# Kernel tuning notes

Hardware: AMD Instinct MI355X
Metric: run time of the kernel (lower is better)

Reference implementation:

```python
import jax, jax.numpy as jnp
import numpy as np

B, S, D, H, DF, L, NC, V, U = 1024, 50, 96, 8, 192, 3, 3, 40000, 5000


def layernorm(x, g, b, eps=1e-5):
    m = jnp.mean(x, axis=-1, keepdims=True)
    v = jnp.mean((x - m) ** 2, axis=-1, keepdims=True)
    return (x - m) * jax.lax.rsqrt(v + eps) * g + b


def gelu(x):
    return jax.nn.gelu(x, approximate=False)  # torch nn.GELU default (erf)


def mha(q, k, v, wi, bi, wo, bo, h):
    # torch nn.MultiheadAttention (batch_first): packed in_proj then out_proj
    d = q.shape[-1]
    dh = d // h
    qp = q @ wi[:d].T + bi[:d]
    kp = k @ wi[d:2 * d].T + bi[d:2 * d]
    vp = v @ wi[2 * d:].T + bi[2 * d:]
    qh = qp.reshape(qp.shape[0], qp.shape[1], h, dh)
    kh = kp.reshape(kp.shape[0], kp.shape[1], h, dh)
    vh = vp.reshape(vp.shape[0], vp.shape[1], h, dh)
    s = jnp.einsum('bqhd,bkhd->bhqk', qh, kh) * (1.0 / np.sqrt(dh)).astype(np.float32)
    a = jax.nn.softmax(s, axis=-1)
    o = jnp.einsum('bhqk,bkhd->bqhd', a, vh).reshape(qp.shape[0], qp.shape[1], d)
    return o @ wo.T + bo


def setup_inputs():
    key = jax.random.key(0)
    ks = iter(jax.random.split(key, 64))

    def p(shape, s=0.02):
        return jax.random.normal(next(ks), shape, jnp.float32) * s

    inp = {
        'locations': jax.random.randint(next(ks), (B, S), 0, V),
        'users': jax.random.randint(next(ks), (B, S), 0, U),
        'start_mins': jax.random.randint(next(ks), (B, S), 0, 1440),
        'weekdays': jax.random.randint(next(ks), (B, S), 0, 7),
        'loc_emb': p((V, D)), 'user_emb': p((U, D)),
        'hour_emb': p((24, D // 4)), 'wd_emb': p((7, D // 4)),
        'temp_w': p((D, D // 2)), 'temp_b': jnp.zeros((D,), jnp.float32),
        'pos_embed': p((1, S, D)), 'init_hidden': p((D,)),
        'out_w1': p((D, D)), 'out_b1': jnp.zeros((D,), jnp.float32),
        'out_w2': p((V, D)), 'out_b2': jnp.zeros((V,), jnp.float32),
    }
    for pre in ('sa', 'ci', 'ch'):  # self_attn, cross_attn_input, cross_attn_hidden
        inp[pre + '_wi'] = p((L, 3 * D, D))
        inp[pre + '_bi'] = jnp.zeros((L, 3 * D), jnp.float32)
        inp[pre + '_wo'] = p((L, D, D))
        inp[pre + '_bo'] = jnp.zeros((L, D), jnp.float32)
    inp['ffn_w1'] = p((L, DF, D)); inp['ffn_b1'] = jnp.zeros((L, DF), jnp.float32)
    inp['ffn_w2'] = p((L, D, DF)); inp['ffn_b2'] = jnp.zeros((L, D), jnp.float32)
    inp['gate_w'] = p((L, D, 2 * D)); inp['gate_b'] = jnp.zeros((L, D), jnp.float32)
    for n in ('n1', 'n2', 'n3'):
        inp[n + '_g'] = jnp.ones((L, D), jnp.float32)
        inp[n + '_b'] = jnp.zeros((L, D), jnp.float32)
    return inp


def reference(locations, users, start_mins, weekdays,
              loc_emb, user_emb, hour_emb, wd_emb, temp_w, temp_b,
              pos_embed, init_hidden, out_w1, out_b1, out_w2, out_b2,
              sa_wi, sa_bi, sa_wo, sa_bo, ci_wi, ci_bi, ci_wo, ci_bo,
              ch_wi, ch_bi, ch_wo, ch_bo, ffn_w1, ffn_b1, ffn_w2, ffn_b2,
              gate_w, gate_b, n1_g, n1_b, n2_g, n2_b, n3_g, n3_b):
    b, s = locations.shape
    hours = (start_mins // 60) % 24
    temporal = jnp.concatenate([hour_emb[hours], wd_emb[weekdays]], axis=-1)  # (B,S,D//2)
    x = (loc_emb[locations] + user_emb[users[:, 0]][:, None, :]
         + temporal @ temp_w.T + temp_b + pos_embed[:, :s, :])  # (B,S,D)
    hidden = jnp.broadcast_to(init_hidden, (b, D))
    for _cycle in range(NC):
        for l in range(L):
            attn = mha(x, x, x, sa_wi[l], sa_bi[l], sa_wo[l], sa_bo[l], H)
            a1 = layernorm(attn + x, n1_g[l], n1_b[l])
            he = hidden[:, None, :]  # single-token query (B,1,D)
            c1 = mha(he, a1, a1, ci_wi[l], ci_bi[l], ci_wo[l], ci_bo[l], H)[:, 0]
            c2 = mha(he, he, he, ch_wi[l], ch_bi[l], ch_wo[l], ch_bo[l], H)[:, 0]
            g = jax.nn.sigmoid(jnp.concatenate([c1, c2], axis=-1) @ gate_w[l].T + gate_b[l])
            gated = layernorm(g * c1 + (1.0 - g) * c2 + hidden, n2_g[l], n2_b[l])
            f = gelu(gated @ ffn_w1[l].T + ffn_b1[l]) @ ffn_w2[l].T + ffn_b2[l]
            hidden = layernorm(f + gated, n3_g[l], n3_b[l])
    logits = gelu(hidden @ out_w1.T + out_b1) @ out_w2.T + out_b2  # (B,V)
    return logits
```

## Files before the change

### kernel.cpp

```cpp
#include <hip/hip_runtime.h>
#include <math.h>

#define B_ 1024
#define S_ 50
#define D_ 96
#define H_ 8
#define DH_ 12
#define DF_ 192
#define L_ 3
#define NC_ 3
#define V_ 40000
#define SR_ 4

#define SCR_L 14745600ull
#define KV_L  9830400ull

typedef __attribute__((ext_vector_type(8))) short short8v;
typedef __attribute__((ext_vector_type(4))) float float4v;

__device__ __forceinline__ float dot4f(float4 a, float4 b) {
  return a.x*b.x + a.y*b.y + a.z*b.z + a.w*b.w;
}
__device__ __forceinline__ float geluf(float v) {
  return 0.5f*v*(1.0f + erff(v*0.70710678118654752f));
}

__global__ void k_embed(const int* __restrict__ loc, const int* __restrict__ users,
                        const int* __restrict__ mins, const int* __restrict__ wd,
                        const float* __restrict__ loc_emb, const float* __restrict__ user_emb,
                        const float* __restrict__ hour_emb, const float* __restrict__ wd_emb,
                        const float* __restrict__ temp_w, const float* __restrict__ temp_b,
                        const float* __restrict__ pos, float* __restrict__ x)
{
  int bs = blockIdx.x; int b = bs / S_; int s = bs % S_;
  __shared__ float tmp[48];
  int t = threadIdx.x;
  if (t < 48) {
    int hr = (mins[bs] / 60) % 24;
    int w  = wd[bs];
    tmp[t] = (t < 24) ? hour_emb[hr*24 + t] : wd_emb[w*24 + (t-24)];
  }
  __syncthreads();
  int lc = loc[bs]; int u = users[b*S_];
  float acc = temp_b[t] + loc_emb[(size_t)lc*D_ + t] + user_emb[(size_t)u*D_ + t] + pos[s*D_ + t];
  const float* twr = temp_w + t*48;
  #pragma unroll
  for (int k = 0; k < 48; k++) acc += tmp[k] * twr[k];
  x[(size_t)bs*D_ + t] = acc;
}

__global__ void k_init(const float* __restrict__ init_hidden, float* __restrict__ hidden) {
  int i = blockIdx.x*256 + threadIdx.x;
  if (i < B_*D_) hidden[i] = init_hidden[i % D_];
}

__global__ void k_tobf16(const float* __restrict__ in, unsigned short* __restrict__ out, int n) {
  int i = blockIdx.x*256 + threadIdx.x;
  if (i < n) {
    unsigned int b = __float_as_uint(in[i]);
    unsigned int r = (b + 0x7FFFu + ((b >> 16) & 1u)) >> 16;
    out[i] = (unsigned short)r;
  }
}

__global__ __launch_bounds__(256) void k_qkv_mfma(const unsigned short* __restrict__ xb,
                                                  const unsigned short* __restrict__ wib,
                                                  const float* __restrict__ bi_b,
                                                  float* __restrict__ qkv)
{
  int l = blockIdx.y;
  const unsigned short* wi = wib + (size_t)l*288*96;
  const float* bi = bi_b + (size_t)l*288;
  float* out = qkv + (size_t)l*SCR_L;

  int tid = threadIdx.x;
  int wv = tid >> 6, lane = tid & 63;
  int c = lane & 15, g = lane >> 4;
  int row0 = blockIdx.x*64 + wv*16;

  short8v afrag[3];
  const unsigned short* arow = xb + (size_t)(row0 + c)*96 + g*8;
  #pragma unroll
  for (int kc = 0; kc < 3; kc++) afrag[kc] = *(const short8v*)&arow[kc*32];

  for (int ct = 0; ct < 18; ct++) {
    int col0 = ct*16;
    short8v bfrag[3];
    const unsigned short* wrow = wi + (size_t)(col0 + c)*96 + g*8;
    #pragma unroll
    for (int kc = 0; kc < 3; kc++) bfrag[kc] = *(const short8v*)&wrow[kc*32];
    float4v acc = {0.f, 0.f, 0.f, 0.f};
    #pragma unroll
    for (int kc = 0; kc < 3; kc++)
      acc = __builtin_amdgcn_mfma_f32_16x16x32_bf16(afrag[kc], bfrag[kc], acc, 0, 0, 0);
    float bj = bi[col0 + c];
    #pragma unroll
    for (int reg = 0; reg < 4; reg++)
      out[(size_t)(row0 + g*4 + reg)*288 + col0 + c] = acc[reg] + bj;
  }
}

__global__ __launch_bounds__(256) void k_attn3(float* __restrict__ qkv)
{
  qkv += (size_t)blockIdx.y*SCR_L;
  __shared__ float q_s[S_*49], k_s[S_*49], v_s[S_*49];
  int tid = threadIdx.x;
  int bh = blockIdx.x; int b = bh >> 1, h4 = bh & 1;
  size_t base = (size_t)b*S_*288 + h4*48;

  for (int idx = tid; idx < 3*S_*12; idx += 256) {
    int m = idx / 600, rem = idx % 600, s = rem / 12, f = rem % 12;
    float4 v = *(const float4*)&qkv[base + (size_t)s*288 + m*96 + 4*f];
    float* dst = (m == 0) ? q_s : (m == 1) ? k_s : v_s;
    dst[s*49 + 4*f+0] = v.x;
    dst[s*49 + 4*f+1] = v.y;
    dst[s*49 + 4*f+2] = v.z;
    dst[s*49 + 4*f+3] = v.w;
  }
  __syncthreads();
  if (tid < 4*S_) {
    int hh = tid / S_, i = tid % S_;
    float q[DH_];
    #pragma unroll
    for (int d = 0; d < DH_; d++) q[d] = q_s[i*49 + hh*12 + d];
    float p[S_]; float mx = -1e30f;
    for (int s = 0; s < S_; s++) {
      const float* kr = &k_s[s*49 + hh*12];
      float acc = 0.f;
      #pragma unroll
      for (int d = 0; d < DH_; d++) acc += q[d]*kr[d];
      acc *= 0.28867513459481287f;
      p[s] = acc; mx = fmaxf(mx, acc);
    }
    float sum = 0.f;
    for (int s = 0; s < S_; s++) { p[s] = expf(p[s] - mx); sum += p[s]; }
    float inv = 1.f / sum;
    float o[DH_];
    #pragma unroll
    for (int d = 0; d < DH_; d++) o[d] = 0.f;
    for (int s = 0; s < S_; s++) {
      const float* vr = &v_s[s*49 + hh*12];
      float pv = p[s];
      #pragma unroll
      for (int d = 0; d < DH_; d++) o[d] += pv*vr[d];
    }
    float* orow = qkv + (size_t)(b*S_ + i)*288 + h4*48 + hh*12;
    #pragma unroll
    for (int d = 0; d < DH_; d++) orow[d] = o[d]*inv;
  }
}

__global__ __launch_bounds__(256) void k_woLNkv(
    const float* __restrict__ A, int lda,
    const float* __restrict__ xres,
    const float* __restrict__ wo, const float* __restrict__ bo,
    const float* __restrict__ n1g, const float* __restrict__ n1b,
    const float* __restrict__ kwi, const float* __restrict__ kbi,
    float* __restrict__ kv)
{
  int l = blockIdx.y;
  A   += (size_t)l*SCR_L;
  wo  += (size_t)l*96*96;  bo  += (size_t)l*96;
  n1g += (size_t)l*96;     n1b += (size_t)l*96;
  kwi += (size_t)l*288*96; kbi += (size_t)l*288;
  kv  += (size_t)l*KV_L;
  __shared__ __align__(16) float lds[15488];
  float* a_t   = lds;
  float* w_t   = lds + 6144;
  float* out_s = lds + 6144;
  float* meanr = lds + 15360;
  float* rstdr = lds + 15424;
  int tid = threadIdx.x;
  int row0 = blockIdx.x*64;
  int tc = tid & 15, tr = tid >> 4;

  for (int idx = tid; idx < 24*64; idx += 256) {
    int kc = idx >> 6, j = idx & 63;
    float4 v = *(const float4*)&A[(size_t)(row0 + j)*lda + 4*kc];
    a_t[(4*kc+0)*64 + j] = v.x;
    a_t[(4*kc+1)*64 + j] = v.y;
    a_t[(4*kc+2)*64 + j] = v.z;
    a_t[(4*kc+3)*64 + j] = v.w;
  }
  for (int idx = tid; idx < 24*96; idx += 256) {
    int kc = idx / 96, j = idx % 96;
    float4 v = *(const float4*)&wo[(size_t)j*96 + 4*kc];
    w_t[(4*kc+0)*96 + j] = v.x;
    w_t[(4*kc+1)*96 + j] = v.y;
    w_t[(4*kc+2)*96 + j] = v.z;
    w_t[(4*kc+3)*96 + j] = v.w;
  }
  __syncthreads();

  float acc[4][6];
  #pragma unroll
  for (int cc = 0; cc < 6; cc++) {
    float bv = bo[tc + 16*cc];
    #pragma unroll
    for (int rr = 0; rr < 4; rr++) acc[rr][cc] = bv;
  }
  #pragma unroll 4
  for (int k = 0; k < 96; k++) {
    float4 av = *(float4*)&a_t[k*64 + 4*tr];
    float a4[4] = {av.x, av.y, av.z, av.w};
    float w6[6];
    #pragma unroll
    for (int cc = 0; cc < 6; cc++) w6[cc] = w_t[k*96 + tc + 16*cc];
    #pragma unroll
    for (int rr = 0; rr < 4; rr++)
      #pragma unroll
      for (int cc = 0; cc < 6; cc++)
        acc[rr][cc] += a4[rr]*w6[cc];
  }
  __syncthreads();

  #pragma unroll
  for (int rr = 0; rr < 4; rr++) {
    int r = 4*tr + rr;
    const float* xr = xres + (size_t)(row0 + r)*96;
    #pragma unroll
    for (int cc = 0; cc < 6; cc++) {
      int j = tc + 16*cc;
      out_s[r*97 + j] = acc[rr][cc] + xr[j];
    }
  }
  __syncthreads();

  if (tid < 64) {
    int r = tid;
    float s1 = 0.f, s2 = 0.f;
    #pragma unroll 8
    for (int j = 0; j < 96; j++) { float v = out_s[r*97 + j]; s1 += v; s2 += v*v; }
    float mean = s1*(1.f/96.f);
    float var = s2*(1.f/96.f) - mean*mean;
    meanr[r] = mean;
    rstdr[r] = rsqrtf(var + 1e-5f);
  }
  __syncthreads();

  for (int idx = tid; idx < 24*64; idx += 256) {
    int kc = idx >> 6, r = idx & 63;
    float mean = meanr[r], rstd = rstdr[r];
    #pragma unroll
    for (int e = 0; e < 4; e++) {
      int k = 4*kc + e;
      float v = (out_s[r*97 + k] - mean)*rstd*n1g[k] + n1b[k];
      a_t[k*64 + r] = v;
    }
  }

  for (int c = 0; c < 3; c++) {
    __syncthreads();
    for (int idx = tid; idx < 24*64; idx += 256) {
      int kc = idx >> 6, j = idx & 63;
      float4 v = *(const float4*)&kwi[(size_t)(64*c + j)*96 + 4*kc];
      w_t[(4*kc+0)*64 + j] = v.x;
      w_t[(4*kc+1)*64 + j] = v.y;
      w_t[(4*kc+2)*64 + j] = v.z;
      w_t[(4*kc+3)*64 + j] = v.w;
    }
    __syncthreads();
    float acc2[4][4];
    #pragma unroll
    for (int cc = 0; cc < 4; cc++) {
      float bv = kbi[64*c + 4*tc + cc];
      #pragma unroll
      for (int rr = 0; rr < 4; rr++) acc2[rr][cc] = bv;
    }
    #pragma unroll 4
    for (int k = 0; k < 96; k++) {
      float4 av = *(float4*)&a_t[k*64 + 4*tr];
      float4 wv = *(float4*)&w_t[k*64 + 4*tc];
      float a4[4] = {av.x, av.y, av.z, av.w};
      float w4[4] = {wv.x, wv.y, wv.z, wv.w};
      #pragma unroll
      for (int rr = 0; rr < 4; rr++)
        #pragma unroll
        for (int cc = 0; cc < 4; cc++)
          acc2[rr][cc] += a4[rr]*w4[cc];
    }
    #pragma unroll
    for (int rr = 0; rr < 4; rr++) {
      int row = row0 + 4*tr + rr;
      float4 o = make_float4(acc2[rr][0], acc2[rr][1], acc2[rr][2], acc2[rr][3]);
      *(float4*)&kv[(size_t)row*192 + 64*c + 4*tc] = o;
    }
  }
}

template<int ACT>
__global__ __launch_bounds__(256) void k_gemm96(const float* __restrict__ A,
                                                const float* __restrict__ W,
                                                const float* __restrict__ bias,
                                                float* __restrict__ out,
                                                int nrows, int out_dim)
{
  __shared__ __align__(16) float a_s[32*100];
  __shared__ __align__(16) float w_s[128*100];
  __shared__ float b_s[128];
  int tid = threadIdx.x;
  int row0 = blockIdx.x*32, col0 = blockIdx.y*128;
  for (int idx = tid; idx < 32*24; idx += 256) {
    int r = idx/24, q = idx%24;
    *(float4*)&a_s[r*100 + q*4] = *(const float4*)&A[(size_t)(row0+r)*96 + q*4];
  }
  for (int idx = tid; idx < 128*24; idx += 256) {
    int j = idx/24, q = idx%24;
    int jj = col0 + j;
    float4 w;
    if (jj < out_dim) w = *(const float4*)&W[(size_t)jj*96 + q*4];
    else { w.x = w.y = w.z = w.w = 0.f; }
    *(float4*)&w_s[j*100 + q*4] = w;
  }
  if (tid < 128) b_s[tid] = (col0 + tid < out_dim) ? bias[col0 + tid] : 0.f;
  __syncthreads();
  int tc = tid % 32, tr = tid / 32;
  int r0 = tr*4;
  float acc[4][4];
  #pragma unroll
  for (int cc = 0; cc < 4; cc++) {
    float bv = b_s[tc + 32*cc];
    #pragma unroll
    for (int rr = 0; rr < 4; rr++) acc[rr][cc] = bv;
  }
  #pragma unroll
  for (int d = 0; d < 96; d += 4) {
    float4 a4[4], w4[4];
    #pragma unroll
    for (int rr = 0; rr < 4; rr++) a4[rr] = *(float4*)&a_s[(r0+rr)*100 + d];
    #pragma unroll
    for (int cc = 0; cc < 4; cc++) w4[cc] = *(float4*)&w_s[(tc + 32*cc)*100 + d];
    #pragma unroll
    for (int rr = 0; rr < 4; rr++)
      #pragma unroll
      for (int cc = 0; cc < 4; cc++)
        acc[rr][cc] += dot4f(a4[rr], w4[cc]);
  }
  #pragma unroll
  for (int rr = 0; rr < 4; rr++) {
    int row = row0 + r0 + rr;
    float* orow = out + (size_t)row*out_dim + col0;
    #pragma unroll
    for (int cc = 0; cc < 4; cc++) {
      int j = tc + 32*cc;
      if (col0 + j < out_dim) {
        float v = acc[rr][cc];
        if (ACT == 1) v = geluf(v);
        orow[j] = v;
      }
    }
  }
}

__global__ __launch_bounds__(256) void k_logits_mfma(const unsigned short* __restrict__ Ab,
                                                     const unsigned short* __restrict__ Wb,
                                                     const float* __restrict__ bias,
                                                     float* __restrict__ out)
{
  int tid = threadIdx.x;
  int wv = tid >> 6, lane = tid & 63;
  int col0 = blockIdx.x*64 + wv*16;
  int c = lane & 15, g = lane >> 4;

  short8v bfrag[3];
  const unsigned short* wrow = Wb + (size_t)(col0 + c)*96 + g*8;
  #pragma unroll
  for (int kc = 0; kc < 3; kc++)
    bfrag[kc] = *(const short8v*)&wrow[kc*32];
  float bj = bias[col0 + c];

  for (int rt = 0; rt < 64; rt++) {
    const unsigned short* arow = Ab + (size_t)(rt*16 + c)*96 + g*8;
    float4v acc = {0.f, 0.f, 0.f, 0.f};
    #pragma unroll
    for (int kc = 0; kc < 3; kc++) {
      short8v afrag = *(const short8v*)&arow[kc*32];
      acc = __builtin_amdgcn_mfma_f32_16x16x32_bf16(afrag, bfrag[kc], acc, 0, 0, 0);
    }
    int row = rt*16 + g*4;
    #pragma unroll
    for (int reg = 0; reg < 4; reg++)
      out[(size_t)(row + reg)*V_ + col0 + c] = acc[reg] + bj;
  }
}

__global__ __launch_bounds__(256) void k_step(float* __restrict__ hidden,
    const float* __restrict__ kv_l,
    const float* __restrict__ ci_wi, const float* __restrict__ ci_bi,
    const float* __restrict__ ci_wo, const float* __restrict__ ci_bo,
    const float* __restrict__ ch_wi, const float* __restrict__ ch_bi,
    const float* __restrict__ ch_wo, const float* __restrict__ ch_bo,
    const float* __restrict__ gw, const float* __restrict__ gb,
    const float* __restrict__ w1, const float* __restrict__ b1,
    const float* __restrict__ w2, const float* __restrict__ b2,
    const float* __restrict__ n2g, const float* __restrict__ n2b,
    const float* __restrict__ n3g, const float* __restrict__ n3b)
{
  __shared__ __align__(16) float hs[SR_][100];
  __shared__ __align__(16) float bufA[SR_][100];
  __shared__ __align__(16) float bufB[SR_][100];
  __shared__ __align__(16) float bufC[SR_][100];
  __shared__ __align__(16) float f1b[SR_][200];
  int tid = threadIdx.x; int b0 = blockIdx.x*SR_;

  for (int idx = tid; idx < SR_*24; idx += 256) {
    int r = idx/24, q = idx%24;
    *(float4*)&hs[r][q*4] = *(const float4*)&hidden[(size_t)(b0+r)*96 + q*4];
  }
  __syncthreads();

  for (int idx = tid; idx < SR_*192; idx += 256) {
    int r = idx % SR_, j = idx / SR_;
    const float* wr = (j < 96) ? (ci_wi + (size_t)j*96) : (ch_wi + (size_t)(96 + j)*96);
    float acc = (j < 96) ? ci_bi[j] : ch_bi[96 + j];
    #pragma unroll
    for (int d = 0; d < 96; d += 4) {
      float4 a = *(float4*)&hs[r][d];
      float4 w = *(const float4*)&wr[d];
      acc += dot4f(a, w);
    }
    if (j < 96) bufA[r][j] = acc; else bufB[r][j-96] = acc;
  }
  __syncthreads();

  if (tid < SR_*8) {
    int r = tid >> 3, h = tid & 7;
    int b = b0 + r;
    float q[12];
    #pragma unroll
    for (int d = 0; d < 12; d++) q[d] = bufA[r][h*12 + d];
    float p[50]; float mx = -1e30f;
    for (int s = 0; s < 50; s++) {
      const float* kr = kv_l + ((size_t)(b*50 + s))*192 + h*12;
      float4 k0 = *(const float4*)&kr[0];
      float4 k1 = *(const float4*)&kr[4];
      float4 k2 = *(const float4*)&kr[8];
      float acc = q[0]*k0.x + q[1]*k0.y + q[2]*k0.z + q[3]*k0.w
                + q[4]*k1.x + q[5]*k1.y + q[6]*k1.z + q[7]*k1.w
                + q[8]*k2.x + q[9]*k2.y + q[10]*k2.z + q[11]*k2.w;
      acc *= 0.28867513459481287f;
      p[s] = acc; mx = fmaxf(mx, acc);
    }
    float sum = 0.f;
    for (int s = 0; s < 50; s++) { p[s] = expf(p[s] - mx); sum += p[s]; }
    float inv = 1.f / sum;
    float o[12];
    #pragma unroll
    for (int d = 0; d < 12; d++) o[d] = 0.f;
    for (int s = 0; s < 50; s++) {
      const float* vr = kv_l + ((size_t)(b*50 + s))*192 + 96 + h*12;
      float4 v0 = *(const float4*)&vr[0];
      float4 v1 = *(const float4*)&vr[4];
      float4 v2 = *(const float4*)&vr[8];
      float pv = p[s];
      o[0] += pv*v0.x; o[1] += pv*v0.y; o[2]  += pv*v0.z; o[3]  += pv*v0.w;
      o[4] += pv*v1.x; o[5] += pv*v1.y; o[6]  += pv*v1.z; o[7]  += pv*v1.w;
      o[8] += pv*v2.x; o[9] += pv*v2.y; o[10] += pv*v2.z; o[11] += pv*v2.w;
    }
    #pragma unroll
    for (int d = 0; d < 12; d++) bufC[r][h*12 + d] = o[d]*inv;
  }
  __syncthreads();

  for (int idx = tid; idx < SR_*192; idx += 256) {
    int r = idx % SR_, j = idx / SR_;
    int jj = (j < 96) ? j : (j - 96);
    const float* ar = (j < 96) ? bufC[r] : bufB[r];
    const float* wr = ((j < 96) ? ci_wo : ch_wo) + (size_t)jj*96;
    float acc = (j < 96) ? ci_bo[jj] : ch_bo[jj];
    #pragma unroll
    for (int d = 0; d < 96; d += 4) {
      float4 a = *(float4*)&ar[d];
      float4 w = *(const float4*)&wr[d];
      acc += dot4f(a, w);
    }
    if (j < 96) bufA[r][j] = acc; else f1b[r][jj] = acc;
  }
  __syncthreads();

  for (int idx = tid; idx < SR_*96; idx += 256) {
    int r = idx % SR_, j = idx / SR_;
    const float* gr = gw + (size_t)j*192;
    float acc = gb[j];
    #pragma unroll
    for (int d = 0; d < 96; d += 4) {
      float4 c1v = *(float4*)&bufA[r][d];
      float4 g1 = *(const float4*)&gr[d];
      float4 c2v = *(float4*)&f1b[r][d];
      float4 g2 = *(const float4*)&gr[96 + d];
      acc += dot4f(c1v, g1) + dot4f(c2v, g2);
    }
    float gv = 1.f/(1.f + expf(-acc));
    float pre = gv*bufA[r][j] + (1.f - gv)*f1b[r][j] + hs[r][j];
    bufB[r][j] = pre;
  }
  __syncthreads();
  if (tid < SR_*16) {
    int r = tid / 16, l16 = tid % 16;
    float s1 = 0.f, s2 = 0.f;
    #pragma unroll
    for (int e = 0; e < 6; e++) { float v = bufB[r][l16*6 + e]; s1 += v; s2 += v*v; }
    for (int off = 8; off > 0; off >>= 1) { s1 += __shfl_xor(s1, off, 16); s2 += __shfl_xor(s2, off, 16); }
    float mean = s1*(1.f/96.f);
    float var = s2*(1.f/96.f) - mean*mean;
    float rstd = rsqrtf(var + 1e-5f);
    #pragma unroll
    for (int e = 0; e < 6; e++) {
      int j = l16*6 + e;
      bufB[r][j] = (bufB[r][j] - mean)*rstd*n2g[j] + n2b[j];
    }
  }
  __syncthreads();

  for (int idx = tid; idx < SR_*192; idx += 256) {
    int r = idx % SR_, j = idx / SR_;
    const float* wr = w1 + (size_t)j*96;
    float acc = b1[j];
    #pragma unroll
    for (int d = 0; d < 96; d += 4) {
      float4 a = *(float4*)&bufB[r][d];
      float4 w = *(const float4*)&wr[d];
      acc += dot4f(a, w);
    }
    f1b[r][j] = geluf(acc);
  }
  __syncthreads();

  for (int idx = tid; idx < SR_*96; idx += 256) {
    int r = idx % SR_, j = idx / SR_;
    const float* wr = w2 + (size_t)j*192;
    float acc = b2[j];
    #pragma unroll
    for (int d = 0; d < 192; d += 4) {
      float4 a = *(float4*)&f1b[r][d];
      float4 w = *(const float4*)&wr[d];
      acc += dot4f(a, w);
    }
    bufC[r][j] = acc + bufB[r][j];
  }
  __syncthreads();
  if (tid < SR_*16) {
    int r = tid / 16, l16 = tid % 16;
    float s1 = 0.f, s2 = 0.f;
    #pragma unroll
    for (int e = 0; e < 6; e++) { float v = bufC[r][l16*6 + e]; s1 += v; s2 += v*v; }
    for (int off = 8; off > 0; off >>= 1) { s1 += __shfl_xor(s1, off, 16); s2 += __shfl_xor(s2, off, 16); }
    float mean = s1*(1.f/96.f);
    float var = s2*(1.f/96.f) - mean*mean;
    float rstd = rsqrtf(var + 1e-5f);
    #pragma unroll
    for (int e = 0; e < 6; e++) {
      int j = l16*6 + e;
      hidden[(size_t)(b0 + r)*96 + j] = (bufC[r][j] - mean)*rstd*n3g[j] + n3b[j];
    }
  }
}

extern "C" void kernel_launch(void* const* d_in, const int* in_sizes, int n_in,
                              void* d_out, int out_size, void* d_ws, size_t ws_size,
                              hipStream_t stream) {
  (void)in_sizes; (void)n_in; (void)out_size; (void)ws_size;
  const int* locations   = (const int*)d_in[0];
  const int* users       = (const int*)d_in[1];
  const int* start_mins  = (const int*)d_in[2];
  const int* weekdays    = (const int*)d_in[3];
  const float* loc_emb   = (const float*)d_in[4];
  const float* user_emb  = (const float*)d_in[5];
  const float* hour_emb  = (const float*)d_in[6];
  const float* wd_emb    = (const float*)d_in[7];
  const float* temp_w    = (const float*)d_in[8];
  const float* temp_b    = (const float*)d_in[9];
  const float* pos_embed = (const float*)d_in[10];
  const float* init_hidden = (const float*)d_in[11];
  const float* out_w1    = (const float*)d_in[12];
  const float* out_b1    = (const float*)d_in[13];
  const float* out_w2    = (const float*)d_in[14];
  const float* out_b2    = (const float*)d_in[15];
  const float* sa_wi = (const float*)d_in[16];
  const float* sa_bi = (const float*)d_in[17];
  const float* sa_wo = (const float*)d_in[18];
  const float* sa_bo = (const float*)d_in[19];
  const float* ci_wi = (const float*)d_in[20];
  const float* ci_bi = (const float*)d_in[21];
  const float* ci_wo = (const float*)d_in[22];
  const float* ci_bo = (const float*)d_in[23];
  const float* ch_wi = (const float*)d_in[24];
  const float* ch_bi = (const float*)d_in[25];
  const float* ch_wo = (const float*)d_in[26];
  const float* ch_bo = (const float*)d_in[27];
  const float* ffn_w1 = (const float*)d_in[28];
  const float* ffn_b1 = (const float*)d_in[29];
  const float* ffn_w2 = (const float*)d_in[30];
  const float* ffn_b2 = (const float*)d_in[31];
  const float* gate_w = (const float*)d_in[32];
  const float* gate_b = (const float*)d_in[33];
  const float* n1_g = (const float*)d_in[34];
  const float* n1_b = (const float*)d_in[35];
  const float* n2_g = (const float*)d_in[36];
  const float* n2_b = (const float*)d_in[37];
  const float* n3_g = (const float*)d_in[38];
  const float* n3_b = (const float*)d_in[39];

  float* ws = (float*)d_ws;
  float* x       = ws;
  float* scratch = x + 4915200;
  float* kv      = scratch + 3ull*SCR_L;
  float* hidden  = kv + 29491200;
  float* h1      = hidden + 98304;

  unsigned short* xb2 = (unsigned short*)kv;
  unsigned short* wib = xb2 + 4915200;
  unsigned short* h1b = (unsigned short*)scratch;
  unsigned short* w2b = h1b + 98304;

  k_embed<<<B_*S_, 96, 0, stream>>>(locations, users, start_mins, weekdays,
                                    loc_emb, user_emb, hour_emb, wd_emb,
                                    temp_w, temp_b, pos_embed, x);
  k_init<<<(B_*D_ + 255)/256, 256, 0, stream>>>(init_hidden, hidden);

  k_tobf16<<<(B_*S_*D_ + 255)/256, 256, 0, stream>>>(x, xb2, B_*S_*D_);
  k_tobf16<<<(3*288*96 + 255)/256, 256, 0, stream>>>(sa_wi, wib, 3*288*96);
  k_qkv_mfma<<<dim3(800, 3), 256, 0, stream>>>(xb2, wib, sa_bi, scratch);
  k_attn3<<<dim3(2048, 3), 256, 0, stream>>>(scratch);
  k_woLNkv<<<dim3(800, 3), 256, 0, stream>>>(scratch, 288, x,
      sa_wo, sa_bo, n1_g, n1_b, ci_wi + 96*96, ci_bi + 96, kv);

  for (int c = 0; c < NC_; c++) {
    for (int l = 0; l < L_; l++) {
      k_step<<<B_/SR_, 256, 0, stream>>>(hidden, kv + (size_t)l*KV_L,
          ci_wi + (size_t)l*288*96, ci_bi + l*288,
          ci_wo + (size_t)l*96*96,  ci_bo + l*96,
          ch_wi + (size_t)l*288*96, ch_bi + l*288,
          ch_wo + (size_t)l*96*96,  ch_bo + l*96,
          gate_w + (size_t)l*96*192, gate_b + l*96,
          ffn_w1 + (size_t)l*192*96, ffn_b1 + l*192,
          ffn_w2 + (size_t)l*96*192, ffn_b2 + l*96,
          n2_g + l*96, n2_b + l*96, n3_g + l*96, n3_b + l*96);
    }
  }

  k_gemm96<1><<<dim3(B_/32, 1), 256, 0, stream>>>(hidden, out_w1, out_b1, h1, B_, 96);
  k_tobf16<<<(B_*D_ + 255)/256, 256, 0, stream>>>(h1, h1b, B_*D_);
  k_tobf16<<<(V_*D_ + 255)/256, 256, 0, stream>>>(out_w2, w2b, V_*D_);
  k_logits_mfma<<<V_/64, 256, 0, stream>>>(h1b, w2b, out_b2, (float*)d_out);
}
```

Measured before the change: 823.6 us.

## Split fused out-proj/LayerNorm/KV kernel into bf16 MFMA stages

Replaces the fused fp32 FMA kernel (self-attention out-projection, residual, LayerNorm, cross-attention K/V projection) with a chain of small kernels. Attention output is converted to bf16 in place, the out-projection and K/V projection run on bf16 MFMA 16x16x32 instructions, and LayerNorm is done with wave shuffles into a bf16 buffer. The aim is to move the GEMM work off scalar FP32 FMAs onto matrix cores. In exchange it adds extra global round trips through scratch, more launches, and bf16 rounding error.

New measurement: 788.1 us. 1.05x faster.

```diff
diff --git a/kernel.cpp b/kernel.cpp
--- a/kernel.cpp
+++ b/kernel.cpp
@@ -24,6 +24,10 @@
 __device__ __forceinline__ float geluf(float v) {
   return 0.5f*v*(1.0f + erff(v*0.70710678118654752f));
 }
+__device__ __forceinline__ unsigned short f2bf(float f) {
+  unsigned int b = __float_as_uint(f);
+  return (unsigned short)((b + 0x7FFFu + ((b >> 16) & 1u)) >> 16);
+}
 
 __global__ void k_embed(const int* __restrict__ loc, const int* __restrict__ users,
                         const int* __restrict__ mins, const int* __restrict__ wd,
@@ -56,11 +60,15 @@
 
 __global__ void k_tobf16(const float* __restrict__ in, unsigned short* __restrict__ out, int n) {
   int i = blockIdx.x*256 + threadIdx.x;
-  if (i < n) {
-    unsigned int b = __float_as_uint(in[i]);
-    unsigned int r = (b + 0x7FFFu + ((b >> 16) & 1u)) >> 16;
-    out[i] = (unsigned short)r;
-  }
+  if (i < n) out[i] = f2bf(in[i]);
+}
+
+__global__ void k_tobf16_attn(float* __restrict__ scratch_base) {
+  float* scr = scratch_base + (size_t)blockIdx.y*SCR_L;
+  int idx = blockIdx.x*256 + threadIdx.x;
+  int row = idx / 96, col = idx % 96;
+  float v = scr[(size_t)row*288 + col];
+  ((unsigned short*)scr)[(size_t)row*576 + 192 + col] = f2bf(v);
 }
 
 __global__ __launch_bounds__(256) void k_qkv_mfma(const unsigned short* __restrict__ xb,
@@ -150,141 +158,108 @@
   }
 }
 
-__global__ __launch_bounds__(256) void k_woLNkv(
-    const float* __restrict__ A, int lda,
-    const float* __restrict__ xres,
-    const float* __restrict__ wo, const float* __restrict__ bo,
-    const float* __restrict__ n1g, const float* __restrict__ n1b,
-    const float* __restrict__ kwi, const float* __restrict__ kbi,
-    float* __restrict__ kv)
+__global__ __launch_bounds__(256) void k_wo_mfma(float* __restrict__ scratch_base,
+                                                 const unsigned short* __restrict__ wo_b,
+                                                 const float* __restrict__ bo_b,
+                                                 const float* __restrict__ x)
 {
   int l = blockIdx.y;
-  A   += (size_t)l*SCR_L;
-  wo  += (size_t)l*96*96;  bo  += (size_t)l*96;
-  n1g += (size_t)l*96;     n1b += (size_t)l*96;
-  kwi += (size_t)l*288*96; kbi += (size_t)l*288;
-  kv  += (size_t)l*KV_L;
-  __shared__ __align__(16) float lds[15488];
-  float* a_t   = lds;
-  float* w_t   = lds + 6144;
-  float* out_s = lds + 6144;
-  float* meanr = lds + 15360;
-  float* rstdr = lds + 15424;
+  float* scr = scratch_base + (size_t)l*SCR_L;
+  const unsigned short* Ab = (const unsigned short*)scr;
+  const unsigned short* wb = wo_b + (size_t)l*96*96;
+  const float* bo = bo_b + (size_t)l*96;
+
   int tid = threadIdx.x;
-  int row0 = blockIdx.x*64;
-  int tc = tid & 15, tr = tid >> 4;
-
-  for (int idx = tid; idx < 24*64; idx += 256) {
-    int kc = idx >> 6, j = idx & 63;
-    float4 v = *(const float4*)&A[(size_t)(row0 + j)*lda + 4*kc];
-    a_t[(4*kc+0)*64 + j] = v.x;
-    a_t[(4*kc+1)*64 + j] = v.y;
-    a_t[(4*kc+2)*64 + j] = v.z;
-    a_t[(4*kc+3)*64 + j] = v.w;
-  }
-  for (int idx = tid; idx < 24*96; idx += 256) {
-    int kc = idx / 96, j = idx % 96;
-    float4 v = *(const float4*)&wo[(size_t)j*96 + 4*kc];
-    w_t[(4*kc+0)*96 + j] = v.x;
-    w_t[(4*kc+1)*96 + j] = v.y;
-    w_t[(4*kc+2)*96 + j] = v.z;
-    w_t[(4*kc+3)*96 + j] = v.w;
-  }
-  __syncthreads();
-
-  float acc[4][6];
-  #pragma unroll
-  for (int cc = 0; cc < 6; cc++) {
-    float bv = bo[tc + 16*cc];
-    #pragma unroll
-    for (int rr = 0; rr < 4; rr++) acc[rr][cc] = bv;
-  }
-  #pragma unroll 4
-  for (int k = 0; k < 96; k++) {
-    float4 av = *(float4*)&a_t[k*64 + 4*tr];
-    float a4[4] = {av.x, av.y, av.z, av.w};
-    float w6[6];
-    #pragma unroll
-    for (int cc = 0; cc < 6; cc++) w6[cc] = w_t[k*96 + tc + 16*cc];
-    #pragma unroll
-    for (int rr = 0; rr < 4; rr++)
-      #pragma unroll
-      for (int cc = 0; cc < 6; cc++)
-        acc[rr][cc] += a4[rr]*w6[cc];
-  }
-  __syncthreads();
-
-  #pragma unroll
-  for (int rr = 0; rr < 4; rr++) {
-    int r = 4*tr + rr;
-    const float* xr = xres + (size_t)(row0 + r)*96;
-    #pragma unroll
-    for (int cc = 0; cc < 6; cc++) {
-      int j = tc + 16*cc;
-      out_s[r*97 + j] = acc[rr][cc] + xr[j];
-    }
-  }
-  __syncthreads();
-
-  if (tid < 64) {
-    int r = tid;
-    float s1 = 0.f, s2 = 0.f;
-    #pragma unroll 8
-    for (int j = 0; j < 96; j++) { float v = out_s[r*97 + j]; s1 += v; s2 += v*v; }
-    float mean = s1*(1.f/96.f);
-    float var = s2*(1.f/96.f) - mean*mean;
-    meanr[r] = mean;
-    rstdr[r] = rsqrtf(var + 1e-5f);
-  }
-  __syncthreads();
-
-  for (int idx = tid; idx < 24*64; idx += 256) {
-    int kc = idx >> 6, r = idx & 63;
-    float mean = meanr[r], rstd = rstdr[r];
-    #pragma unroll
-    for (int e = 0; e < 4; e++) {
-      int k = 4*kc + e;
-      float v = (out_s[r*97 + k] - mean)*rstd*n1g[k] + n1b[k];
-      a_t[k*64 + r] = v;
-    }
-  }
-
-  for (int c = 0; c < 3; c++) {
-    __syncthreads();
-    for (int idx = tid; idx < 24*64; idx += 256) {
-      int kc = idx >> 6, j = idx & 63;
-      float4 v = *(const float4*)&kwi[(size_t)(64*c + j)*96 + 4*kc];
-      w_t[(4*kc+0)*64 + j] = v.x;
-      w_t[(4*kc+1)*64 + j] = v.y;
-      w_t[(4*kc+2)*64 + j] = v.z;
-      w_t[(4*kc+3)*64 + j] = v.w;
-    }
-    __syncthreads();
-    float acc2[4][4];
-    #pragma unroll
-    for (int cc = 0; cc < 4; cc++) {
-      float bv = kbi[64*c + 4*tc + cc];
-      #pragma unroll
-      for (int rr = 0; rr < 4; rr++) acc2[rr][cc] = bv;
-    }
-    #pragma unroll 4
-    for (int k = 0; k < 96; k++) {
-      float4 av = *(float4*)&a_t[k*64 + 4*tr];
-      float4 wv = *(float4*)&w_t[k*64 + 4*tc];
-      float a4[4] = {av.x, av.y, av.z, av.w};
-      float w4[4] = {wv.x, wv.y, wv.z, wv.w};
-      #pragma unroll
-      for (int rr = 0; rr < 4; rr++)
-        #pragma unroll
-        for (int cc = 0; cc < 4; cc++)
-          acc2[rr][cc] += a4[rr]*w4[cc];
-    }
-    #pragma unroll
-    for (int rr = 0; rr < 4; rr++) {
-      int row = row0 + 4*tr + rr;
-      float4 o = make_float4(acc2[rr][0], acc2[rr][1], acc2[rr][2], acc2[rr][3]);
-      *(float4*)&kv[(size_t)row*192 + 64*c + 4*tc] = o;
-    }
+  int wv = tid >> 6, lane = tid & 63;
+  int c = lane & 15, g = lane >> 4;
+  int row0 = blockIdx.x*64 + wv*16;
+
+  short8v afrag[3];
+  const unsigned short* arow = Ab + (size_t)(row0 + c)*576 + 192 + g*8;
+  #pragma unroll
+  for (int kc = 0; kc < 3; kc++) afrag[kc] = *(const short8v*)&arow[kc*32];
+
+  for (int ct = 0; ct < 6; ct++) {
+    int col0 = ct*16;
+    short8v bfrag[3];
+    const unsigned short* wrow = wb + (size_t)(col0 + c)*96 + g*8;
+    #pragma unroll
+    for (int kc = 0; kc < 3; kc++) bfrag[kc] = *(const short8v*)&wrow[kc*32];
+    float4v acc = {0.f, 0.f, 0.f, 0.f};
+    #pragma unroll
+    for (int kc = 0; kc < 3; kc++)
+      acc = __builtin_amdgcn_mfma_f32_16x16x32_bf16(afrag[kc], bfrag[kc], acc, 0, 0, 0);
+    float bj = bo[col0 + c];
+    #pragma unroll
+    for (int reg = 0; reg < 4; reg++) {
+      int row = row0 + g*4 + reg;
+      scr[(size_t)row*288 + 144 + col0 + c] = acc[reg] + bj + x[(size_t)row*96 + col0 + c];
+    }
+  }
+}
+
+__global__ __launch_bounds__(256) void k_lnbf16(float* __restrict__ scratch_base,
+                                                const float* __restrict__ n1g_b,
+                                                const float* __restrict__ n1b_b)
+{
+  int l = blockIdx.y;
+  float* scr = scratch_base + (size_t)l*SCR_L;
+  const float* g = n1g_b + (size_t)l*96;
+  const float* bb = n1b_b + (size_t)l*96;
+  int row = blockIdx.x*4 + (threadIdx.x >> 6);
+  int t = threadIdx.x & 63;
+  const float* in = scr + (size_t)row*288 + 144;
+  float e0 = in[t];
+  float e1 = (t < 32) ? in[64 + t] : 0.f;
+  float s = e0 + e1;
+  for (int off = 32; off > 0; off >>= 1) s += __shfl_xor(s, off, 64);
+  float mean = s * (1.f/96.f);
+  float d0 = e0 - mean;
+  float d1 = (t < 32) ? (e1 - mean) : 0.f;
+  float v = d0*d0 + d1*d1;
+  for (int off = 32; off > 0; off >>= 1) v += __shfl_xor(v, off, 64);
+  float rstd = rsqrtf(v*(1.f/96.f) + 1e-5f);
+  unsigned short* outp = (unsigned short*)scr + (size_t)row*576 + 480;
+  outp[t] = f2bf(d0*rstd*g[t] + bb[t]);
+  if (t < 32) outp[64 + t] = f2bf(d1*rstd*g[64 + t] + bb[64 + t]);
+}
+
+__global__ __launch_bounds__(256) void k_kv_mfma(const float* __restrict__ scratch_base,
+                                                 const unsigned short* __restrict__ kwi_full,
+                                                 const float* __restrict__ ci_bi_b,
+                                                 float* __restrict__ kv_base)
+{
+  int l = blockIdx.y;
+  const float* scr = scratch_base + (size_t)l*SCR_L;
+  const unsigned short* Ab = (const unsigned short*)scr;
+  const unsigned short* kwi = kwi_full + (size_t)l*288*96 + 96*96;
+  const float* kbi = ci_bi_b + (size_t)l*288 + 96;
+  float* out = kv_base + (size_t)l*KV_L;
+
+  int tid = threadIdx.x;
+  int wv = tid >> 6, lane = tid & 63;
+  int c = lane & 15, g = lane >> 4;
+  int row0 = blockIdx.x*64 + wv*16;
+
+  short8v afrag[3];
+  const unsigned short* arow = Ab + (size_t)(row0 + c)*576 + 480 + g*8;
+  #pragma unroll
+  for (int kc = 0; kc < 3; kc++) afrag[kc] = *(const short8v*)&arow[kc*32];
+
+  for (int ct = 0; ct < 12; ct++) {
+    int col0 = ct*16;
+    short8v bfrag[3];
+    const unsigned short* wrow = kwi + (size_t)(col0 + c)*96 + g*8;
+    #pragma unroll
+    for (int kc = 0; kc < 3; kc++) bfrag[kc] = *(const short8v*)&wrow[kc*32];
+    float4v acc = {0.f, 0.f, 0.f, 0.f};
+    #pragma unroll
+    for (int kc = 0; kc < 3; kc++)
+      acc = __builtin_amdgcn_mfma_f32_16x16x32_bf16(afrag[kc], bfrag[kc], acc, 0, 0, 0);
+    float bj = kbi[col0 + c];
+    #pragma unroll
+    for (int reg = 0; reg < 4; reg++)
+      out[(size_t)(row0 + g*4 + reg)*192 + col0 + c] = acc[reg] + bj;
   }
 }
 
@@ -610,6 +585,8 @@
 
   unsigned short* xb2 = (unsigned short*)kv;
   unsigned short* wib = xb2 + 4915200;
+  unsigned short* wo_b  = (unsigned short*)h1;
+  unsigned short* kwi_b = wo_b + 27648;
   unsigned short* h1b = (unsigned short*)scratch;
   unsigned short* w2b = h1b + 98304;
 
@@ -620,10 +597,14 @@
 
   k_tobf16<<<(B_*S_*D_ + 255)/256, 256, 0, stream>>>(x, xb2, B_*S_*D_);
   k_tobf16<<<(3*288*96 + 255)/256, 256, 0, stream>>>(sa_wi, wib, 3*288*96);
+  k_tobf16<<<(3*96*96 + 255)/256, 256, 0, stream>>>(sa_wo, wo_b, 3*96*96);
+  k_tobf16<<<(3*288*96 + 255)/256, 256, 0, stream>>>(ci_wi, kwi_b, 3*288*96);
   k_qkv_mfma<<<dim3(800, 3), 256, 0, stream>>>(xb2, wib, sa_bi, scratch);
   k_attn3<<<dim3(2048, 3), 256, 0, stream>>>(scratch);
-  k_woLNkv<<<dim3(800, 3), 256, 0, stream>>>(scratch, 288, x,
-      sa_wo, sa_bo, n1_g, n1_b, ci_wi + 96*96, ci_bi + 96, kv);
+  k_tobf16_attn<<<dim3(19200, 3), 256, 0, stream>>>(scratch);
+  k_wo_mfma<<<dim3(800, 3), 256, 0, stream>>>(scratch, wo_b, sa_bo, x);
+  k_lnbf16<<<dim3(12800, 3), 256, 0, stream>>>(scratch, n1_g, n1_b);
+  k_kv_mfma<<<dim3(800, 3), 256, 0, stream>>>(scratch, kwi_b, ci_bi, kv);
 
   for (int c = 0; c < NC_; c++) {
     for (int l = 0; l < L_; l++) {
```
